# Optimization experiments

Measured on AMD Instinct MI355X. Metric: run time of the kernel, lower is better.

The kernel has to match this reference:

```python
import jax, jax.numpy as jnp
import numpy as np

B, S, D = 8, 1024, 768
H, HD = 12, 64  # heads, head dim (H*HD == D)
EPS = 1e-12


def setup_inputs() -> dict:
    key = jax.random.key(0)
    ks = jax.random.split(key, 8)
    s = 0.02
    return {
        "hidden_states": jax.random.normal(ks[0], (B, S, D), jnp.float32),
        "attention_mask": jnp.zeros((B, 1, 1, S), jnp.float32),
        "head_mask": jnp.ones((H,), jnp.float32),
        "Wq": jax.random.normal(ks[1], (D, H * HD), jnp.float32) * s,
        "bq": jnp.zeros((H * HD,), jnp.float32),
        "Wk": jax.random.normal(ks[2], (D, H * HD), jnp.float32) * s,
        "bk": jnp.zeros((H * HD,), jnp.float32),
        "Wv": jax.random.normal(ks[3], (D, H * HD), jnp.float32) * s,
        "bv": jnp.zeros((H * HD,), jnp.float32),
        "Wo": jax.random.normal(ks[4], (D, H * HD), jnp.float32) * s,  # torch Linear weight [out=D, in=H*HD]
        "bo": jnp.zeros((D,), jnp.float32),
        "gamma": jnp.ones((D,), jnp.float32),
        "beta": jnp.zeros((D,), jnp.float32),
    }


def reference(hidden_states, attention_mask, head_mask, Wq, bq, Wk, bk, Wv, bv, Wo, bo, gamma, beta):
    def heads(x):  # [B,S,H*HD] -> [B,H,S,HD]
        return x.reshape(B, S, H, HD).transpose(0, 2, 1, 3)

    q = heads(hidden_states @ Wq.T + bq)
    k = heads(hidden_states @ Wk.T + bk)
    v = heads(hidden_states @ Wv.T + bv)

    scores = jnp.einsum("bhqd,bhkd->bhqk", q, k) / np.sqrt(HD).astype(np.float32)
    scores = scores + attention_mask
    probs = jax.nn.softmax(scores, axis=-1)  # dropout p=0 (eval)
    ctx = jnp.einsum("bhqk,bhkd->bhqd", probs, v)  # [B,H,S,HD]

    # masked per-head output projection: Wo.T.view(H, HD, D)
    Wph = Wo.T.reshape(H, HD, D)
    proj = jnp.einsum("bhsd,hde,h->bse", ctx, Wph, head_mask) + bo

    # residual + LayerNorm
    x = proj + hidden_states
    mu = jnp.mean(x, axis=-1, keepdims=True)
    var = jnp.mean(jnp.square(x - mu), axis=-1, keepdims=True)
    out = (x - mu) * jax.lax.rsqrt(var + EPS) * gamma + beta
    return out
```

## Files before the change

### kernel.cpp

```cpp
#include <hip/hip_runtime.h>
#include <math.h>

#define Bn 8
#define Sn 1024
#define Dn 768
#define Hn 12
#define MROWS (Bn * Sn)

typedef __attribute__((ext_vector_type(8))) short short8;
typedef __attribute__((ext_vector_type(4))) float floatx4;

__device__ __forceinline__ unsigned short f2b(float x) {
    union { float f; unsigned u; } v; v.f = x;
    unsigned r = v.u + 0x7fffu + ((v.u >> 16) & 1u);
    return (unsigned short)(r >> 16);
}

__device__ __forceinline__ void gload16(const void* g, void* l) {
    __builtin_amdgcn_global_load_lds(
        (const __attribute__((address_space(1))) void*)g,
        (__attribute__((address_space(3))) void*)l, 16, 0, 0);
}

__global__ __launch_bounds__(256) void convert_all(const float* __restrict__ X,
                                                   const float* __restrict__ Wq, const float* __restrict__ Wk,
                                                   const float* __restrict__ Wv, const float* __restrict__ Wo,
                                                   unsigned short* __restrict__ Xb,
                                                   unsigned short* __restrict__ Wqb, unsigned short* __restrict__ Wkb,
                                                   unsigned short* __restrict__ Wvb, unsigned short* __restrict__ Wob) {
    const int id = blockIdx.x;
    const float* src;
    unsigned short* dst;
    int i;
    if (id < 6144) {
        src = X; dst = Xb;
        i = id * 256 + threadIdx.x;
    } else {
        const int y = (id - 6144) / 576;
        src = (y == 0) ? Wq : (y == 1) ? Wk : (y == 2) ? Wv : Wo;
        dst = (y == 0) ? Wqb : (y == 1) ? Wkb : (y == 2) ? Wvb : Wob;
        i = ((id - 6144) % 576) * 256 + threadIdx.x;
    }
    float4 v = reinterpret_cast<const float4*>(src)[i];
    ushort4 o;
    o.x = f2b(v.x); o.y = f2b(v.y); o.z = f2b(v.z); o.w = f2b(v.w);
    reinterpret_cast<ushort4*>(dst)[i] = o;
}

__global__ __launch_bounds__(256) void gemm_qkv(const unsigned short* __restrict__ A,
                                                const unsigned short* __restrict__ Wq,
                                                const unsigned short* __restrict__ Wk,
                                                const unsigned short* __restrict__ Wv,
                                                const float* __restrict__ bq,
                                                const float* __restrict__ bk,
                                                const float* __restrict__ bv,
                                                unsigned short* __restrict__ Qh,
                                                unsigned short* __restrict__ Kh,
                                                unsigned short* __restrict__ Vt) {
    __shared__ __align__(16) unsigned short As[2][128 * 32];
    __shared__ __align__(16) unsigned short Ws[2][128 * 32];
    const int id = blockIdx.x;
    const int by = id & 63;
    const int bx = id >> 6;
    const int mat = bx / 6;
    const int m0 = by * 128;
    const int n0 = (bx % 6) * 128;
    const unsigned short* W = (mat == 0) ? Wq : (mat == 1) ? Wk : Wv;
    const float* bias = (mat == 0) ? bq : (mat == 1) ? bk : bv;
    unsigned short* Cout = (mat == 0) ? Qh : (mat == 1) ? Kh : Vt;

    const int tid = threadIdx.x;
    const int w = tid >> 6, l = tid & 63, quad = l >> 4, mr = l & 15;
    const int wm = (w >> 1) * 64, wn = (w & 1) * 64;

    const unsigned short* gA0 = &A[(size_t)(m0 + w * 32 + (l >> 2)) * Dn + (l & 3) * 8];
    const unsigned short* gA1 = gA0 + 16 * Dn;
    const unsigned short* gW0 = &W[(size_t)(n0 + w * 32 + (l >> 2)) * Dn + (l & 3) * 8];
    const unsigned short* gW1 = gW0 + 16 * Dn;
    const int lo = w * 1024;

    floatx4 acc[4][4];
#pragma unroll
    for (int i = 0; i < 4; i++)
#pragma unroll
        for (int j = 0; j < 4; j++) {
            floatx4 z = {0.f, 0.f, 0.f, 0.f};
            acc[i][j] = z;
        }

    gload16(gA0, &As[0][lo]);
    gload16(gA1, &As[0][lo + 512]);
    gload16(gW0, &Ws[0][lo]);
    gload16(gW1, &Ws[0][lo + 512]);

    for (int kt = 0; kt < 24; kt++) {
        const int cur = kt & 1;
        __syncthreads();
        if (kt < 23) {
            const int k0 = (kt + 1) * 32;
            const int nxt = cur ^ 1;
            gload16(gA0 + k0, &As[nxt][lo]);
            gload16(gA1 + k0, &As[nxt][lo + 512]);
            gload16(gW0 + k0, &Ws[nxt][lo]);
            gload16(gW1 + k0, &Ws[nxt][lo + 512]);
        }
        short8 af[4], bfr[4];
#pragma unroll
        for (int i = 0; i < 4; i++)
            af[i] = *(const short8*)&As[cur][(wm + i * 16 + mr) * 32 + quad * 8];
#pragma unroll
        for (int j = 0; j < 4; j++)
            bfr[j] = *(const short8*)&Ws[cur][(wn + j * 16 + mr) * 32 + quad * 8];
#pragma unroll
        for (int i = 0; i < 4; i++)
#pragma unroll
            for (int j = 0; j < 4; j++)
                acc[i][j] = __builtin_amdgcn_mfma_f32_16x16x32_bf16(af[i], bfr[j], acc[i][j], 0, 0, 0);
    }

#pragma unroll
    for (int j = 0; j < 4; j++) {
        const int col = n0 + wn + j * 16 + mr;
        const float bval = bias[col];
        const int h = col >> 6, d = col & 63;
#pragma unroll
        for (int i = 0; i < 4; i++) {
#pragma unroll
            for (int r = 0; r < 4; r++) {
                const int m = m0 + wm + i * 16 + quad * 4 + r;
                const float val = acc[i][j][r] + bval;
                const int b = m >> 10, s = m & 1023;
                const size_t base = (size_t)(b * Hn + h) << 16;
                if (mat == 2)
                    Cout[base + (size_t)d * 1024 + s] = f2b(val);
                else
                    Cout[base + (size_t)s * 64 + d] = f2b(val);
            }
        }
    }
}

__global__ __launch_bounds__(256) void gemm_out(const unsigned short* __restrict__ A,
                                                const unsigned short* __restrict__ W,
                                                const float* __restrict__ bias,
                                                const float* __restrict__ X,
                                                float* __restrict__ xres) {
    __shared__ __align__(16) unsigned short As[2][64 * 32];
    __shared__ __align__(16) unsigned short Ws[2][128 * 32];
    const int id = blockIdx.x;
    const int by = id & 127;
    const int bx = id >> 7;
    const int m0 = by * 64;
    const int n0 = bx * 128;

    const int tid = threadIdx.x;
    const int w = tid >> 6, l = tid & 63, quad = l >> 4, mr = l & 15;

    const unsigned short* gA0 = &A[(size_t)(m0 + w * 16 + (l >> 2)) * Dn + (l & 3) * 8];
    const unsigned short* gW0 = &W[(size_t)(n0 + w * 32 + (l >> 2)) * Dn + (l & 3) * 8];
    const unsigned short* gW1 = gW0 + 16 * Dn;
    const int loA = w * 512;
    const int loW = w * 1024;

    floatx4 acc[4][2];
#pragma unroll
    for (int i = 0; i < 4; i++)
#pragma unroll
        for (int j = 0; j < 2; j++) {
            floatx4 z = {0.f, 0.f, 0.f, 0.f};
            acc[i][j] = z;
        }

    gload16(gA0, &As[0][loA]);
    gload16(gW0, &Ws[0][loW]);
    gload16(gW1, &Ws[0][loW + 512]);

    for (int kt = 0; kt < 24; kt++) {
        const int cur = kt & 1;
        __syncthreads();
        if (kt < 23) {
            const int k0 = (kt + 1) * 32;
            const int nxt = cur ^ 1;
            gload16(gA0 + k0, &As[nxt][loA]);
            gload16(gW0 + k0, &Ws[nxt][loW]);
            gload16(gW1 + k0, &Ws[nxt][loW + 512]);
        }
        short8 af[4], bfr[2];
#pragma unroll
        for (int i = 0; i < 4; i++)
            af[i] = *(const short8*)&As[cur][(i * 16 + mr) * 32 + quad * 8];
#pragma unroll
        for (int j = 0; j < 2; j++)
            bfr[j] = *(const short8*)&Ws[cur][(w * 32 + j * 16 + mr) * 32 + quad * 8];
#pragma unroll
        for (int i = 0; i < 4; i++)
#pragma unroll
            for (int j = 0; j < 2; j++)
                acc[i][j] = __builtin_amdgcn_mfma_f32_16x16x32_bf16(af[i], bfr[j], acc[i][j], 0, 0, 0);
    }

#pragma unroll
    for (int j = 0; j < 2; j++) {
        const int col = n0 + w * 32 + j * 16 + mr;
        const float bval = bias[col];
#pragma unroll
        for (int i = 0; i < 4; i++) {
#pragma unroll
            for (int r = 0; r < 4; r++) {
                const int m = m0 + i * 16 + quad * 4 + r;
                xres[(size_t)m * Dn + col] = acc[i][j][r] + bval + X[(size_t)m * Dn + col];
            }
        }
    }
}

__global__ __launch_bounds__(256) void flash_attn_mfma(const unsigned short* __restrict__ Qh,
                                                       const unsigned short* __restrict__ Kh,
                                                       const unsigned short* __restrict__ Vt,
                                                       const float* __restrict__ mask,
                                                       const float* __restrict__ head_mask,
                                                       unsigned short* __restrict__ ctx) {
    __shared__ __align__(16) unsigned short Ks[64 * 72];
    __shared__ __align__(16) unsigned short Vs[64 * 72];
    __shared__ __align__(16) unsigned short Ps[128 * 72];
    __shared__ float msk[64];

    const int id = blockIdx.x;
    const int bh = id % 96;
    const int qt = id / 96;
    const int b = bh / Hn, h = bh % Hn;
    const int q0 = qt * 128;
    const int tid = threadIdx.x;
    const int w = tid >> 6, l = tid & 63, quad = l >> 4, mr = l & 15;
    const size_t hb = (size_t)(b * Hn + h) << 16;

    short8 aq[2][2];
#pragma unroll
    for (int i = 0; i < 2; i++)
#pragma unroll
        for (int ks = 0; ks < 2; ks++)
            aq[i][ks] = *(const short8*)&Qh[hb + (size_t)(q0 + w * 32 + i * 16 + mr) * 64 + ks * 32 + quad * 8];

    float l_s[2][4];
    floatx4 oacc[2][4];
#pragma unroll
    for (int i = 0; i < 2; i++) {
#pragma unroll
        for (int r = 0; r < 4; r++) l_s[i][r] = 0.f;
#pragma unroll
        for (int jj = 0; jj < 4; jj++) {
            floatx4 z = {0.f, 0.f, 0.f, 0.f};
            oacc[i][jj] = z;
        }
    }

    const int srow = tid >> 2;
    const int scol = (tid & 3) * 16;

    short8 pk0 = *(const short8*)&Kh[hb + (size_t)srow * 64 + scol];
    short8 pk1 = *(const short8*)&Kh[hb + (size_t)srow * 64 + scol + 8];
    short8 pv0 = *(const short8*)&Vt[hb + (size_t)srow * 1024 + scol];
    short8 pv1 = *(const short8*)&Vt[hb + (size_t)srow * 1024 + scol + 8];
    float pm = mask[b * Sn + (tid & 63)];

    for (int kt = 0; kt < Sn / 64; kt++) {
        __syncthreads();
        *(short8*)&Ks[srow * 72 + scol] = pk0;
        *(short8*)&Ks[srow * 72 + scol + 8] = pk1;
        *(short8*)&Vs[srow * 72 + scol] = pv0;
        *(short8*)&Vs[srow * 72 + scol + 8] = pv1;
        if (tid < 64) msk[tid] = pm;
        if (kt < Sn / 64 - 1) {
            const int k0 = (kt + 1) * 64;
            pk0 = *(const short8*)&Kh[hb + (size_t)(k0 + srow) * 64 + scol];
            pk1 = *(const short8*)&Kh[hb + (size_t)(k0 + srow) * 64 + scol + 8];
            pv0 = *(const short8*)&Vt[hb + (size_t)srow * 1024 + k0 + scol];
            pv1 = *(const short8*)&Vt[hb + (size_t)srow * 1024 + k0 + scol + 8];
            pm = mask[b * Sn + k0 + (tid & 63)];
        }
        __syncthreads();

        floatx4 sacc[2][4];
#pragma unroll
        for (int i = 0; i < 2; i++)
#pragma unroll
            for (int j = 0; j < 4; j++) {
                floatx4 z = {0.f, 0.f, 0.f, 0.f};
                sacc[i][j] = z;
            }
#pragma unroll
        for (int ks = 0; ks < 2; ks++) {
#pragma unroll
            for (int j = 0; j < 4; j++) {
                short8 bk = *(const short8*)&Ks[(j * 16 + mr) * 72 + ks * 32 + quad * 8];
                sacc[0][j] = __builtin_amdgcn_mfma_f32_16x16x32_bf16(aq[0][ks], bk, sacc[0][j], 0, 0, 0);
                sacc[1][j] = __builtin_amdgcn_mfma_f32_16x16x32_bf16(aq[1][ks], bk, sacc[1][j], 0, 0, 0);
            }
        }

#pragma unroll
        for (int i = 0; i < 2; i++) {
#pragma unroll
            for (int j = 0; j < 4; j++) {
                const float mk = msk[j * 16 + mr];
#pragma unroll
                for (int r = 0; r < 4; r++) {
                    const float p = __expf(sacc[i][j][r] * 0.125f + mk);
                    l_s[i][r] += p;
                    Ps[(w * 32 + i * 16 + quad * 4 + r) * 72 + j * 16 + mr] = f2b(p);
                }
            }
        }

#pragma unroll
        for (int ks = 0; ks < 2; ks++) {
            short8 ap0 = *(const short8*)&Ps[(w * 32 + mr) * 72 + ks * 32 + quad * 8];
            short8 ap1 = *(const short8*)&Ps[(w * 32 + 16 + mr) * 72 + ks * 32 + quad * 8];
#pragma unroll
            for (int jj = 0; jj < 4; jj++) {
                short8 bv = *(const short8*)&Vs[(jj * 16 + mr) * 72 + ks * 32 + quad * 8];
                oacc[0][jj] = __builtin_amdgcn_mfma_f32_16x16x32_bf16(ap0, bv, oacc[0][jj], 0, 0, 0);
                oacc[1][jj] = __builtin_amdgcn_mfma_f32_16x16x32_bf16(ap1, bv, oacc[1][jj], 0, 0, 0);
            }
        }
    }

    const float hm = head_mask[h];
    float inv[2][4];
#pragma unroll
    for (int i = 0; i < 2; i++)
#pragma unroll
        for (int r = 0; r < 4; r++) {
            float t = l_s[i][r];
            t += __shfl_xor(t, 1);
            t += __shfl_xor(t, 2);
            t += __shfl_xor(t, 4);
            t += __shfl_xor(t, 8);
            inv[i][r] = hm / t;
        }
#pragma unroll
    for (int i = 0; i < 2; i++)
#pragma unroll
        for (int jj = 0; jj < 4; jj++)
#pragma unroll
            for (int r = 0; r < 4; r++) {
                const int qrow = q0 + w * 32 + i * 16 + quad * 4 + r;
                ctx[(size_t)(b * Sn + qrow) * Dn + h * 64 + jj * 16 + mr] = f2b(oacc[i][jj][r] * inv[i][r]);
            }
}

__global__ __launch_bounds__(256) void ln_kernel(const float* __restrict__ x,
                                                 const float* __restrict__ gamma,
                                                 const float* __restrict__ beta,
                                                 float* __restrict__ out) {
    __shared__ float r1[256];
    __shared__ float r2[256];
    const int m = blockIdx.x;
    const int tid = threadIdx.x;

    float xv[3];
    float s = 0.f, ss = 0.f;
#pragma unroll
    for (int i = 0; i < 3; i++) {
        int j = tid + i * 256;
        float t = x[(size_t)m * Dn + j];
        xv[i] = t;
        s += t;
        ss += t * t;
    }
    r1[tid] = s;
    r2[tid] = ss;
    __syncthreads();
    for (int off = 128; off > 0; off >>= 1) {
        if (tid < off) {
            r1[tid] += r1[tid + off];
            r2[tid] += r2[tid + off];
        }
        __syncthreads();
    }
    const float mu = r1[0] * (1.0f / Dn);
    const float var = r2[0] * (1.0f / Dn) - mu * mu;
    const float rstd = rsqrtf(var + 1e-12f);
#pragma unroll
    for (int i = 0; i < 3; i++) {
        int j = tid + i * 256;
        out[(size_t)m * Dn + j] = (xv[i] - mu) * rstd * gamma[j] + beta[j];
    }
}

extern "C" void kernel_launch(void* const* d_in, const int* in_sizes, int n_in,
                              void* d_out, int out_size, void* d_ws, size_t ws_size,
                              hipStream_t stream) {
    const float* X         = (const float*)d_in[0];
    const float* mask      = (const float*)d_in[1];
    const float* head_mask = (const float*)d_in[2];
    const float* Wq        = (const float*)d_in[3];
    const float* bq        = (const float*)d_in[4];
    const float* Wk        = (const float*)d_in[5];
    const float* bk        = (const float*)d_in[6];
    const float* Wv        = (const float*)d_in[7];
    const float* bv        = (const float*)d_in[8];
    const float* Wo        = (const float*)d_in[9];
    const float* bo        = (const float*)d_in[10];
    const float* gamma     = (const float*)d_in[11];
    const float* beta      = (const float*)d_in[12];
    float* out = (float*)d_out;

    const size_t NE = (size_t)Bn * Sn * Dn;
    const size_t NW = (size_t)Dn * Dn;

    char* p = (char*)d_ws;
    unsigned short* Xb  = (unsigned short*)p;  p += NE * 2;
    unsigned short* Wqb = (unsigned short*)p;  p += NW * 2;
    unsigned short* Wkb = (unsigned short*)p;  p += NW * 2;
    unsigned short* Wvb = (unsigned short*)p;  p += NW * 2;
    unsigned short* Wob = (unsigned short*)p;  p += NW * 2;
    unsigned short* Qh  = (unsigned short*)p;  p += NE * 2;
    unsigned short* Kh  = (unsigned short*)p;  p += NE * 2;
    unsigned short* Vtb = (unsigned short*)p;  p += NE * 2;
    unsigned short* ctx = (unsigned short*)p;  p += NE * 2;
    float* xres = (float*)p;

    convert_all<<<8448, 256, 0, stream>>>(X, Wq, Wk, Wv, Wo, Xb, Wqb, Wkb, Wvb, Wob);

    gemm_qkv<<<1152, 256, 0, stream>>>(Xb, Wqb, Wkb, Wvb, bq, bk, bv, Qh, Kh, Vtb);

    flash_attn_mfma<<<768, 256, 0, stream>>>(Qh, Kh, Vtb, mask, head_mask, ctx);

    gemm_out<<<768, 256, 0, stream>>>(ctx, Wob, bo, X, xres);

    ln_kernel<<<MROWS, 256, 0, stream>>>(xres, gamma, beta, out);
}
```

Baseline: 244.4 us.

## Swap MFMA operand order to transpose accumulators for vectorized epilogue stores

Swaps the A/B operands of the MFMA calls in the QKV GEMM, output GEMM and attention kernel, so each lane's four accumulator values lie along the contiguous output dimension. This lets epilogues write packed bf16 pairs (uint2) or float4 instead of scattered scalar stores, and lets attention load the mask as float4 into registers instead of staging it through shared memory. It also adds occupancy hints to launch bounds and uses the hardware bf16x2 conversion. The risk is extra register pressure from the transposed layouts, and possible LDS bank conflicts on the new P-tile store pattern.

```diff
diff --git a/kernel.cpp b/kernel.cpp
--- a/kernel.cpp
+++ b/kernel.cpp
@@ -1,4 +1,5 @@
 #include <hip/hip_runtime.h>
+#include <hip/hip_bf16.h>
 #include <math.h>
 
 #define Bn 8
@@ -14,6 +15,12 @@
     union { float f; unsigned u; } v; v.f = x;
     unsigned r = v.u + 0x7fffu + ((v.u >> 16) & 1u);
     return (unsigned short)(r >> 16);
+}
+
+__device__ __forceinline__ unsigned pk2(float a, float b) {
+    union { __hip_bfloat162 h2; unsigned u; } cv;
+    cv.h2 = __float22bfloat162_rn(float2{a, b});
+    return cv.u;
 }
 
 __device__ __forceinline__ void gload16(const void* g, void* l) {
@@ -47,16 +54,16 @@
     reinterpret_cast<ushort4*>(dst)[i] = o;
 }
 
-__global__ __launch_bounds__(256) void gemm_qkv(const unsigned short* __restrict__ A,
-                                                const unsigned short* __restrict__ Wq,
-                                                const unsigned short* __restrict__ Wk,
-                                                const unsigned short* __restrict__ Wv,
-                                                const float* __restrict__ bq,
-                                                const float* __restrict__ bk,
-                                                const float* __restrict__ bv,
-                                                unsigned short* __restrict__ Qh,
-                                                unsigned short* __restrict__ Kh,
-                                                unsigned short* __restrict__ Vt) {
+__global__ __launch_bounds__(256, 4) void gemm_qkv(const unsigned short* __restrict__ A,
+                                                   const unsigned short* __restrict__ Wq,
+                                                   const unsigned short* __restrict__ Wk,
+                                                   const unsigned short* __restrict__ Wv,
+                                                   const float* __restrict__ bq,
+                                                   const float* __restrict__ bk,
+                                                   const float* __restrict__ bv,
+                                                   unsigned short* __restrict__ Qh,
+                                                   unsigned short* __restrict__ Kh,
+                                                   unsigned short* __restrict__ Vt) {
     __shared__ __align__(16) unsigned short As[2][128 * 32];
     __shared__ __align__(16) unsigned short Ws[2][128 * 32];
     const int id = blockIdx.x;
@@ -93,6 +100,7 @@
     gload16(gW0, &Ws[0][lo]);
     gload16(gW1, &Ws[0][lo + 512]);
 
+    const bool swapOrd = (mat != 2);
     for (int kt = 0; kt < 24; kt++) {
         const int cur = kt & 1;
         __syncthreads();
@@ -111,40 +119,61 @@
 #pragma unroll
         for (int j = 0; j < 4; j++)
             bfr[j] = *(const short8*)&Ws[cur][(wn + j * 16 + mr) * 32 + quad * 8];
-#pragma unroll
-        for (int i = 0; i < 4; i++)
-#pragma unroll
-            for (int j = 0; j < 4; j++)
-                acc[i][j] = __builtin_amdgcn_mfma_f32_16x16x32_bf16(af[i], bfr[j], acc[i][j], 0, 0, 0);
-    }
-
-#pragma unroll
-    for (int j = 0; j < 4; j++) {
-        const int col = n0 + wn + j * 16 + mr;
-        const float bval = bias[col];
-        const int h = col >> 6, d = col & 63;
-#pragma unroll
-        for (int i = 0; i < 4; i++) {
-#pragma unroll
-            for (int r = 0; r < 4; r++) {
-                const int m = m0 + wm + i * 16 + quad * 4 + r;
-                const float val = acc[i][j][r] + bval;
+        if (swapOrd) {
+#pragma unroll
+            for (int i = 0; i < 4; i++)
+#pragma unroll
+                for (int j = 0; j < 4; j++)
+                    acc[i][j] = __builtin_amdgcn_mfma_f32_16x16x32_bf16(bfr[j], af[i], acc[i][j], 0, 0, 0);
+        } else {
+#pragma unroll
+            for (int i = 0; i < 4; i++)
+#pragma unroll
+                for (int j = 0; j < 4; j++)
+                    acc[i][j] = __builtin_amdgcn_mfma_f32_16x16x32_bf16(af[i], bfr[j], acc[i][j], 0, 0, 0);
+        }
+    }
+
+    if (swapOrd) {
+#pragma unroll
+        for (int j = 0; j < 4; j++) {
+            const int nb = n0 + wn + j * 16 + quad * 4;
+            const float4 b4 = *(const float4*)&bias[nb];
+            const int h = nb >> 6, d0 = nb & 63;
+#pragma unroll
+            for (int i = 0; i < 4; i++) {
+                const int m = m0 + wm + i * 16 + mr;
                 const int b = m >> 10, s = m & 1023;
-                const size_t base = (size_t)(b * Hn + h) << 16;
-                if (mat == 2)
-                    Cout[base + (size_t)d * 1024 + s] = f2b(val);
-                else
-                    Cout[base + (size_t)s * 64 + d] = f2b(val);
-            }
-        }
-    }
-}
-
-__global__ __launch_bounds__(256) void gemm_out(const unsigned short* __restrict__ A,
-                                                const unsigned short* __restrict__ W,
-                                                const float* __restrict__ bias,
-                                                const float* __restrict__ X,
-                                                float* __restrict__ xres) {
+                uint2 pp;
+                pp.x = pk2(acc[i][j][0] + b4.x, acc[i][j][1] + b4.y);
+                pp.y = pk2(acc[i][j][2] + b4.z, acc[i][j][3] + b4.w);
+                *(uint2*)&Cout[((size_t)(b * Hn + h) << 16) + (size_t)s * 64 + d0] = pp;
+            }
+        }
+    } else {
+#pragma unroll
+        for (int j = 0; j < 4; j++) {
+            const int col = n0 + wn + j * 16 + mr;
+            const float bval = bias[col];
+            const int h = col >> 6, d = col & 63;
+#pragma unroll
+            for (int i = 0; i < 4; i++) {
+                const int mb = m0 + wm + i * 16 + quad * 4;
+                const int b = mb >> 10, s0 = mb & 1023;
+                uint2 pp;
+                pp.x = pk2(acc[i][j][0] + bval, acc[i][j][1] + bval);
+                pp.y = pk2(acc[i][j][2] + bval, acc[i][j][3] + bval);
+                *(uint2*)&Cout[((size_t)(b * Hn + h) << 16) + (size_t)d * 1024 + s0] = pp;
+            }
+        }
+    }
+}
+
+__global__ __launch_bounds__(256, 4) void gemm_out(const unsigned short* __restrict__ A,
+                                                   const unsigned short* __restrict__ W,
+                                                   const float* __restrict__ bias,
+                                                   const float* __restrict__ X,
+                                                   float* __restrict__ xres) {
     __shared__ __align__(16) unsigned short As[2][64 * 32];
     __shared__ __align__(16) unsigned short Ws[2][128 * 32];
     const int id = blockIdx.x;
@@ -196,20 +225,23 @@
         for (int i = 0; i < 4; i++)
 #pragma unroll
             for (int j = 0; j < 2; j++)
-                acc[i][j] = __builtin_amdgcn_mfma_f32_16x16x32_bf16(af[i], bfr[j], acc[i][j], 0, 0, 0);
+                acc[i][j] = __builtin_amdgcn_mfma_f32_16x16x32_bf16(bfr[j], af[i], acc[i][j], 0, 0, 0);
     }
 
 #pragma unroll
     for (int j = 0; j < 2; j++) {
-        const int col = n0 + w * 32 + j * 16 + mr;
-        const float bval = bias[col];
+        const int nb = n0 + w * 32 + j * 16 + quad * 4;
+        const float4 b4 = *(const float4*)&bias[nb];
 #pragma unroll
         for (int i = 0; i < 4; i++) {
-#pragma unroll
-            for (int r = 0; r < 4; r++) {
-                const int m = m0 + i * 16 + quad * 4 + r;
-                xres[(size_t)m * Dn + col] = acc[i][j][r] + bval + X[(size_t)m * Dn + col];
-            }
+            const int m = m0 + i * 16 + mr;
+            const float4 xr = *(const float4*)&X[(size_t)m * Dn + nb];
+            float4 o;
+            o.x = acc[i][j][0] + b4.x + xr.x;
+            o.y = acc[i][j][1] + b4.y + xr.y;
+            o.z = acc[i][j][2] + b4.z + xr.z;
+            o.w = acc[i][j][3] + b4.w + xr.w;
+            *(float4*)&xres[(size_t)m * Dn + nb] = o;
         }
     }
 }
@@ -223,7 +255,6 @@
     __shared__ __align__(16) unsigned short Ks[64 * 72];
     __shared__ __align__(16) unsigned short Vs[64 * 72];
     __shared__ __align__(16) unsigned short Ps[128 * 72];
-    __shared__ float msk[64];
 
     const int id = blockIdx.x;
     const int bh = id % 96;
@@ -234,25 +265,22 @@
     const int w = tid >> 6, l = tid & 63, quad = l >> 4, mr = l & 15;
     const size_t hb = (size_t)(b * Hn + h) << 16;
 
-    short8 aq[2][2];
-#pragma unroll
-    for (int i = 0; i < 2; i++)
+    short8 bq[2][2];
+#pragma unroll
+    for (int n = 0; n < 2; n++)
 #pragma unroll
         for (int ks = 0; ks < 2; ks++)
-            aq[i][ks] = *(const short8*)&Qh[hb + (size_t)(q0 + w * 32 + i * 16 + mr) * 64 + ks * 32 + quad * 8];
-
-    float l_s[2][4];
-    floatx4 oacc[2][4];
-#pragma unroll
-    for (int i = 0; i < 2; i++) {
-#pragma unroll
-        for (int r = 0; r < 4; r++) l_s[i][r] = 0.f;
-#pragma unroll
-        for (int jj = 0; jj < 4; jj++) {
+            bq[n][ks] = *(const short8*)&Qh[hb + (size_t)(q0 + w * 32 + n * 16 + mr) * 64 + ks * 32 + quad * 8];
+
+    float l_acc[2] = {0.f, 0.f};
+    floatx4 oacc[4][2];
+#pragma unroll
+    for (int dt = 0; dt < 4; dt++)
+#pragma unroll
+        for (int n = 0; n < 2; n++) {
             floatx4 z = {0.f, 0.f, 0.f, 0.f};
-            oacc[i][jj] = z;
-        }
-    }
+            oacc[dt][n] = z;
+        }
 
     const int srow = tid >> 2;
     const int scol = (tid & 3) * 16;
@@ -261,7 +289,10 @@
     short8 pk1 = *(const short8*)&Kh[hb + (size_t)srow * 64 + scol + 8];
     short8 pv0 = *(const short8*)&Vt[hb + (size_t)srow * 1024 + scol];
     short8 pv1 = *(const short8*)&Vt[hb + (size_t)srow * 1024 + scol + 8];
-    float pm = mask[b * Sn + (tid & 63)];
+    float4 mm[4];
+#pragma unroll
+    for (int i = 0; i < 4; i++)
+        mm[i] = *(const float4*)&mask[b * Sn + i * 16 + quad * 4];
 
     for (int kt = 0; kt < Sn / 64; kt++) {
         __syncthreads();
@@ -269,84 +300,89 @@
         *(short8*)&Ks[srow * 72 + scol + 8] = pk1;
         *(short8*)&Vs[srow * 72 + scol] = pv0;
         *(short8*)&Vs[srow * 72 + scol + 8] = pv1;
-        if (tid < 64) msk[tid] = pm;
+        float4 cm[4];
+#pragma unroll
+        for (int i = 0; i < 4; i++) cm[i] = mm[i];
         if (kt < Sn / 64 - 1) {
             const int k0 = (kt + 1) * 64;
             pk0 = *(const short8*)&Kh[hb + (size_t)(k0 + srow) * 64 + scol];
             pk1 = *(const short8*)&Kh[hb + (size_t)(k0 + srow) * 64 + scol + 8];
             pv0 = *(const short8*)&Vt[hb + (size_t)srow * 1024 + k0 + scol];
             pv1 = *(const short8*)&Vt[hb + (size_t)srow * 1024 + k0 + scol + 8];
-            pm = mask[b * Sn + k0 + (tid & 63)];
+#pragma unroll
+            for (int i = 0; i < 4; i++)
+                mm[i] = *(const float4*)&mask[b * Sn + k0 + i * 16 + quad * 4];
         }
         __syncthreads();
 
-        floatx4 sacc[2][4];
-#pragma unroll
-        for (int i = 0; i < 2; i++)
-#pragma unroll
-            for (int j = 0; j < 4; j++) {
+        floatx4 sacc[4][2];
+#pragma unroll
+        for (int i = 0; i < 4; i++)
+#pragma unroll
+            for (int n = 0; n < 2; n++) {
                 floatx4 z = {0.f, 0.f, 0.f, 0.f};
-                sacc[i][j] = z;
+                sacc[i][n] = z;
             }
 #pragma unroll
         for (int ks = 0; ks < 2; ks++) {
 #pragma unroll
-            for (int j = 0; j < 4; j++) {
-                short8 bk = *(const short8*)&Ks[(j * 16 + mr) * 72 + ks * 32 + quad * 8];
-                sacc[0][j] = __builtin_amdgcn_mfma_f32_16x16x32_bf16(aq[0][ks], bk, sacc[0][j], 0, 0, 0);
-                sacc[1][j] = __builtin_amdgcn_mfma_f32_16x16x32_bf16(aq[1][ks], bk, sacc[1][j], 0, 0, 0);
-            }
-        }
-
-#pragma unroll
-        for (int i = 0; i < 2; i++) {
-#pragma unroll
-            for (int j = 0; j < 4; j++) {
-                const float mk = msk[j * 16 + mr];
-#pragma unroll
-                for (int r = 0; r < 4; r++) {
-                    const float p = __expf(sacc[i][j][r] * 0.125f + mk);
-                    l_s[i][r] += p;
-                    Ps[(w * 32 + i * 16 + quad * 4 + r) * 72 + j * 16 + mr] = f2b(p);
-                }
+            for (int i = 0; i < 4; i++) {
+                short8 ak = *(const short8*)&Ks[(i * 16 + mr) * 72 + ks * 32 + quad * 8];
+                sacc[i][0] = __builtin_amdgcn_mfma_f32_16x16x32_bf16(ak, bq[0][ks], sacc[i][0], 0, 0, 0);
+                sacc[i][1] = __builtin_amdgcn_mfma_f32_16x16x32_bf16(ak, bq[1][ks], sacc[i][1], 0, 0, 0);
+            }
+        }
+
+#pragma unroll
+        for (int i = 0; i < 4; i++) {
+#pragma unroll
+            for (int n = 0; n < 2; n++) {
+                const float p0 = __expf(sacc[i][n][0] * 0.125f + cm[i].x);
+                const float p1 = __expf(sacc[i][n][1] * 0.125f + cm[i].y);
+                const float p2 = __expf(sacc[i][n][2] * 0.125f + cm[i].z);
+                const float p3 = __expf(sacc[i][n][3] * 0.125f + cm[i].w);
+                l_acc[n] += p0 + p1 + p2 + p3;
+                uint2 pp;
+                pp.x = pk2(p0, p1);
+                pp.y = pk2(p2, p3);
+                *(uint2*)&Ps[(w * 32 + n * 16 + mr) * 72 + i * 16 + quad * 4] = pp;
             }
         }
 
 #pragma unroll
         for (int ks = 0; ks < 2; ks++) {
-            short8 ap0 = *(const short8*)&Ps[(w * 32 + mr) * 72 + ks * 32 + quad * 8];
-            short8 ap1 = *(const short8*)&Ps[(w * 32 + 16 + mr) * 72 + ks * 32 + quad * 8];
-#pragma unroll
-            for (int jj = 0; jj < 4; jj++) {
-                short8 bv = *(const short8*)&Vs[(jj * 16 + mr) * 72 + ks * 32 + quad * 8];
-                oacc[0][jj] = __builtin_amdgcn_mfma_f32_16x16x32_bf16(ap0, bv, oacc[0][jj], 0, 0, 0);
-                oacc[1][jj] = __builtin_amdgcn_mfma_f32_16x16x32_bf16(ap1, bv, oacc[1][jj], 0, 0, 0);
+            short8 bp0 = *(const short8*)&Ps[(w * 32 + mr) * 72 + ks * 32 + quad * 8];
+            short8 bp1 = *(const short8*)&Ps[(w * 32 + 16 + mr) * 72 + ks * 32 + quad * 8];
+#pragma unroll
+            for (int dt = 0; dt < 4; dt++) {
+                short8 av = *(const short8*)&Vs[(dt * 16 + mr) * 72 + ks * 32 + quad * 8];
+                oacc[dt][0] = __builtin_amdgcn_mfma_f32_16x16x32_bf16(av, bp0, oacc[dt][0], 0, 0, 0);
+                oacc[dt][1] = __builtin_amdgcn_mfma_f32_16x16x32_bf16(av, bp1, oacc[dt][1], 0, 0, 0);
             }
         }
     }
 
     const float hm = head_mask[h];
-    float inv[2][4];
-#pragma unroll
-    for (int i = 0; i < 2; i++)
-#pragma unroll
-        for (int r = 0; r < 4; r++) {
-            float t = l_s[i][r];
-            t += __shfl_xor(t, 1);
-            t += __shfl_xor(t, 2);
-            t += __shfl_xor(t, 4);
-            t += __shfl_xor(t, 8);
-            inv[i][r] = hm / t;
-        }
-#pragma unroll
-    for (int i = 0; i < 2; i++)
-#pragma unroll
-        for (int jj = 0; jj < 4; jj++)
-#pragma unroll
-            for (int r = 0; r < 4; r++) {
-                const int qrow = q0 + w * 32 + i * 16 + quad * 4 + r;
-                ctx[(size_t)(b * Sn + qrow) * Dn + h * 64 + jj * 16 + mr] = f2b(oacc[i][jj][r] * inv[i][r]);
-            }
+    float inv[2];
+#pragma unroll
+    for (int n = 0; n < 2; n++) {
+        float t = l_acc[n];
+        t += __shfl_xor(t, 16);
+        t += __shfl_xor(t, 32);
+        inv[n] = hm / t;
+    }
+#pragma unroll
+    for (int n = 0; n < 2; n++) {
+        const int q = q0 + w * 32 + n * 16 + mr;
+        unsigned short* dst = &ctx[(size_t)(b * Sn + q) * Dn + h * 64 + quad * 4];
+#pragma unroll
+        for (int dt = 0; dt < 4; dt++) {
+            uint2 pp;
+            pp.x = pk2(oacc[dt][n][0] * inv[n], oacc[dt][n][1] * inv[n]);
+            pp.y = pk2(oacc[dt][n][2] * inv[n], oacc[dt][n][3] * inv[n]);
+            *(uint2*)&dst[dt * 16] = pp;
+        }
+    }
 }
 
 __global__ __launch_bounds__(256) void ln_kernel(const float* __restrict__ x,
```

After: 402.7 us. 1.65x slower.

## Load GEMM fragments directly from global memory and use wave-shuffle LayerNorm reduction

Applied to the files above, without the earlier changes.

Both projection GEMMs drop their LDS double buffer and barriers. Each lane now loads its MFMA operand fragments straight from global memory into registers, with a one-step register prefetch. This removes LDS traffic and __syncthreads, but each wave now reads its own copy of the tiles, so data is no longer shared across waves and global/L2 traffic rises. The LayerNorm reduction switches from a shared-memory tree with many barriers to wave shuffles plus a single barrier.

```diff
diff --git a/kernel.cpp b/kernel.cpp
--- a/kernel.cpp
+++ b/kernel.cpp
@@ -1,4 +1,5 @@
 #include <hip/hip_runtime.h>
+#include <hip/hip_bf16.h>
 #include <math.h>
 
 #define Bn 8
@@ -14,12 +15,6 @@
     union { float f; unsigned u; } v; v.f = x;
     unsigned r = v.u + 0x7fffu + ((v.u >> 16) & 1u);
     return (unsigned short)(r >> 16);
-}
-
-__device__ __forceinline__ void gload16(const void* g, void* l) {
-    __builtin_amdgcn_global_load_lds(
-        (const __attribute__((address_space(1))) void*)g,
-        (__attribute__((address_space(3))) void*)l, 16, 0, 0);
 }
 
 __global__ __launch_bounds__(256) void convert_all(const float* __restrict__ X,
@@ -57,8 +52,6 @@
                                                 unsigned short* __restrict__ Qh,
                                                 unsigned short* __restrict__ Kh,
                                                 unsigned short* __restrict__ Vt) {
-    __shared__ __align__(16) unsigned short As[2][128 * 32];
-    __shared__ __align__(16) unsigned short Ws[2][128 * 32];
     const int id = blockIdx.x;
     const int by = id & 63;
     const int bx = id >> 6;
@@ -73,11 +66,14 @@
     const int w = tid >> 6, l = tid & 63, quad = l >> 4, mr = l & 15;
     const int wm = (w >> 1) * 64, wn = (w & 1) * 64;
 
-    const unsigned short* gA0 = &A[(size_t)(m0 + w * 32 + (l >> 2)) * Dn + (l & 3) * 8];
-    const unsigned short* gA1 = gA0 + 16 * Dn;
-    const unsigned short* gW0 = &W[(size_t)(n0 + w * 32 + (l >> 2)) * Dn + (l & 3) * 8];
-    const unsigned short* gW1 = gW0 + 16 * Dn;
-    const int lo = w * 1024;
+    const unsigned short* pA[4];
+    const unsigned short* pW[4];
+#pragma unroll
+    for (int i = 0; i < 4; i++)
+        pA[i] = &A[(size_t)(m0 + wm + i * 16 + mr) * Dn + quad * 8];
+#pragma unroll
+    for (int j = 0; j < 4; j++)
+        pW[j] = &W[(size_t)(n0 + wn + j * 16 + mr) * Dn + quad * 8];
 
     floatx4 acc[4][4];
 #pragma unroll
@@ -88,34 +84,28 @@
             acc[i][j] = z;
         }
 
-    gload16(gA0, &As[0][lo]);
-    gload16(gA1, &As[0][lo + 512]);
-    gload16(gW0, &Ws[0][lo]);
-    gload16(gW1, &Ws[0][lo + 512]);
+    short8 af[4], bf[4], naf[4], nbf[4];
+#pragma unroll
+    for (int i = 0; i < 4; i++) af[i] = *(const short8*)pA[i];
+#pragma unroll
+    for (int j = 0; j < 4; j++) bf[j] = *(const short8*)pW[j];
 
     for (int kt = 0; kt < 24; kt++) {
-        const int cur = kt & 1;
-        __syncthreads();
         if (kt < 23) {
-            const int k0 = (kt + 1) * 32;
-            const int nxt = cur ^ 1;
-            gload16(gA0 + k0, &As[nxt][lo]);
-            gload16(gA1 + k0, &As[nxt][lo + 512]);
-            gload16(gW0 + k0, &Ws[nxt][lo]);
-            gload16(gW1 + k0, &Ws[nxt][lo + 512]);
-        }
-        short8 af[4], bfr[4];
+#pragma unroll
+            for (int i = 0; i < 4; i++) naf[i] = *(const short8*)(pA[i] + 32);
+#pragma unroll
+            for (int j = 0; j < 4; j++) nbf[j] = *(const short8*)(pW[j] + 32);
+        }
 #pragma unroll
         for (int i = 0; i < 4; i++)
-            af[i] = *(const short8*)&As[cur][(wm + i * 16 + mr) * 32 + quad * 8];
-#pragma unroll
-        for (int j = 0; j < 4; j++)
-            bfr[j] = *(const short8*)&Ws[cur][(wn + j * 16 + mr) * 32 + quad * 8];
-#pragma unroll
-        for (int i = 0; i < 4; i++)
 #pragma unroll
             for (int j = 0; j < 4; j++)
-                acc[i][j] = __builtin_amdgcn_mfma_f32_16x16x32_bf16(af[i], bfr[j], acc[i][j], 0, 0, 0);
+                acc[i][j] = __builtin_amdgcn_mfma_f32_16x16x32_bf16(af[i], bf[j], acc[i][j], 0, 0, 0);
+#pragma unroll
+        for (int i = 0; i < 4; i++) { af[i] = naf[i]; pA[i] += 32; }
+#pragma unroll
+        for (int j = 0; j < 4; j++) { bf[j] = nbf[j]; pW[j] += 32; }
     }
 
 #pragma unroll
@@ -145,8 +135,6 @@
                                                 const float* __restrict__ bias,
                                                 const float* __restrict__ X,
                                                 float* __restrict__ xres) {
-    __shared__ __align__(16) unsigned short As[2][64 * 32];
-    __shared__ __align__(16) unsigned short Ws[2][128 * 32];
     const int id = blockIdx.x;
     const int by = id & 127;
     const int bx = id >> 7;
@@ -156,11 +144,14 @@
     const int tid = threadIdx.x;
     const int w = tid >> 6, l = tid & 63, quad = l >> 4, mr = l & 15;
 
-    const unsigned short* gA0 = &A[(size_t)(m0 + w * 16 + (l >> 2)) * Dn + (l & 3) * 8];
-    const unsigned short* gW0 = &W[(size_t)(n0 + w * 32 + (l >> 2)) * Dn + (l & 3) * 8];
-    const unsigned short* gW1 = gW0 + 16 * Dn;
-    const int loA = w * 512;
-    const int loW = w * 1024;
+    const unsigned short* pA[4];
+    const unsigned short* pW[2];
+#pragma unroll
+    for (int i = 0; i < 4; i++)
+        pA[i] = &A[(size_t)(m0 + i * 16 + mr) * Dn + quad * 8];
+#pragma unroll
+    for (int j = 0; j < 2; j++)
+        pW[j] = &W[(size_t)(n0 + w * 32 + j * 16 + mr) * Dn + quad * 8];
 
     floatx4 acc[4][2];
 #pragma unroll
@@ -171,32 +162,28 @@
             acc[i][j] = z;
         }
 
-    gload16(gA0, &As[0][loA]);
-    gload16(gW0, &Ws[0][loW]);
-    gload16(gW1, &Ws[0][loW + 512]);
+    short8 af[4], bf[2], naf[4], nbf[2];
+#pragma unroll
+    for (int i = 0; i < 4; i++) af[i] = *(const short8*)pA[i];
+#pragma unroll
+    for (int j = 0; j < 2; j++) bf[j] = *(const short8*)pW[j];
 
     for (int kt = 0; kt < 24; kt++) {
-        const int cur = kt & 1;
-        __syncthreads();
         if (kt < 23) {
-            const int k0 = (kt + 1) * 32;
-            const int nxt = cur ^ 1;
-            gload16(gA0 + k0, &As[nxt][loA]);
-            gload16(gW0 + k0, &Ws[nxt][loW]);
-            gload16(gW1 + k0, &Ws[nxt][loW + 512]);
-        }
-        short8 af[4], bfr[2];
+#pragma unroll
+            for (int i = 0; i < 4; i++) naf[i] = *(const short8*)(pA[i] + 32);
+#pragma unroll
+            for (int j = 0; j < 2; j++) nbf[j] = *(const short8*)(pW[j] + 32);
+        }
 #pragma unroll
         for (int i = 0; i < 4; i++)
-            af[i] = *(const short8*)&As[cur][(i * 16 + mr) * 32 + quad * 8];
-#pragma unroll
-        for (int j = 0; j < 2; j++)
-            bfr[j] = *(const short8*)&Ws[cur][(w * 32 + j * 16 + mr) * 32 + quad * 8];
-#pragma unroll
-        for (int i = 0; i < 4; i++)
 #pragma unroll
             for (int j = 0; j < 2; j++)
-                acc[i][j] = __builtin_amdgcn_mfma_f32_16x16x32_bf16(af[i], bfr[j], acc[i][j], 0, 0, 0);
+                acc[i][j] = __builtin_amdgcn_mfma_f32_16x16x32_bf16(af[i], bf[j], acc[i][j], 0, 0, 0);
+#pragma unroll
+        for (int i = 0; i < 4; i++) { af[i] = naf[i]; pA[i] += 32; }
+#pragma unroll
+        for (int j = 0; j < 2; j++) { bf[j] = nbf[j]; pW[j] += 32; }
     }
 
 #pragma unroll
@@ -353,10 +340,11 @@
                                                  const float* __restrict__ gamma,
                                                  const float* __restrict__ beta,
                                                  float* __restrict__ out) {
-    __shared__ float r1[256];
-    __shared__ float r2[256];
+    __shared__ float r1[4];
+    __shared__ float r2[4];
     const int m = blockIdx.x;
     const int tid = threadIdx.x;
+    const int w = tid >> 6, lane = tid & 63;
 
     float xv[3];
     float s = 0.f, ss = 0.f;
@@ -368,18 +356,17 @@
         s += t;
         ss += t * t;
     }
-    r1[tid] = s;
-    r2[tid] = ss;
+#pragma unroll
+    for (int o = 1; o < 64; o <<= 1) {
+        s += __shfl_xor(s, o);
+        ss += __shfl_xor(ss, o);
+    }
+    if (lane == 0) { r1[w] = s; r2[w] = ss; }
     __syncthreads();
-    for (int off = 128; off > 0; off >>= 1) {
-        if (tid < off) {
-            r1[tid] += r1[tid + off];
-            r2[tid] += r2[tid + off];
-        }
-        __syncthreads();
-    }
-    const float mu = r1[0] * (1.0f / Dn);
-    const float var = r2[0] * (1.0f / Dn) - mu * mu;
+    const float sum = r1[0] + r1[1] + r1[2] + r1[3];
+    const float sqs = r2[0] + r2[1] + r2[2] + r2[3];
+    const float mu = sum * (1.0f / Dn);
+    const float var = sqs * (1.0f / Dn) - mu * mu;
     const float rstd = rsqrtf(var + 1e-12f);
 #pragma unroll
     for (int i = 0; i < 3; i++) {
```

New measurement: 340.1 us. +39.2%, slower.
